# Performance work log

Hardware: AMD Instinct MI355X
Metric: run time of the kernel (lower is better)

Reference implementation:

```python
import jax, jax.numpy as jnp
import numpy as np

BATCH, CHANNELS, WINDOW, N_PATCHES = 16, 64, 200, 30
D_MODEL = 256
HIDDEN = D_MODEL // 2  # 128


def setup_inputs() -> dict:
    key = jax.random.key(0)
    ks = jax.random.split(key, 7)
    s = 1.0 / np.sqrt(HIDDEN)
    return {
        "x": jax.random.normal(ks[0], (BATCH, CHANNELS, WINDOW, N_PATCHES), dtype=jnp.float32),
        "W_ih": jax.random.normal(ks[1], (4 * HIDDEN, CHANNELS), dtype=jnp.float32) * s,
        "W_hh": jax.random.normal(ks[2], (4 * HIDDEN, HIDDEN), dtype=jnp.float32) * s,
        "b_ih": jax.random.normal(ks[3], (4 * HIDDEN,), dtype=jnp.float32) * s,
        "b_hh": jax.random.normal(ks[4], (4 * HIDDEN,), dtype=jnp.float32) * s,
        "W_fc": jax.random.normal(ks[5], (CHANNELS, HIDDEN), dtype=jnp.float32) * s,
        "b_fc": jax.random.normal(ks[6], (CHANNELS,), dtype=jnp.float32) * s,
    }


def _lstm_last_h(x_seq, W_ih, W_hh, b_ih, b_hh):
    # x_seq: (N, T, C) -> final hidden state (N, H). PyTorch gate order: i, f, g, o.
    N = x_seq.shape[0]
    H = W_hh.shape[1]
    # Precompute input contribution for all timesteps: (N, T, 4H)
    xg = jnp.einsum('ntc,gc->ntg', x_seq, W_ih) + b_ih + b_hh
    xg_t = jnp.swapaxes(xg, 0, 1)  # (T, N, 4H)

    def step(carry, xt):
        h, c = carry
        gates = xt + h @ W_hh.T  # (N, 4H)
        i, f, g, o = jnp.split(gates, 4, axis=-1)
        i = jax.nn.sigmoid(i)
        f = jax.nn.sigmoid(f)
        g = jnp.tanh(g)
        o = jax.nn.sigmoid(o)
        c = f * c + i * g
        h = o * jnp.tanh(c)
        return (h, c), None

    h0 = jnp.zeros((N, H), dtype=x_seq.dtype)
    c0 = jnp.zeros((N, H), dtype=x_seq.dtype)
    (h_T, _), _ = jax.lax.scan(step, (h0, c0), xg_t)
    return h_T


def reference(x, W_ih, W_hh, b_ih, b_hh, W_fc, b_fc):
    batch, channels, window, n_patches = x.shape
    # (B, C, T, P) -> (B, P, T, C) -> (B*P, T, C): each patch is an LSTM sequence
    x_flat = jnp.transpose(x, (0, 3, 2, 1)).reshape(batch * n_patches, window, channels)
    h_last = _lstm_last_h(x_flat, W_ih, W_hh, b_ih, b_hh)  # (B*P, H)
    out = h_last @ W_fc.T + b_fc  # (B*P, C)
    return out.reshape(batch, n_patches, channels)
```

## Files before the change

### kernel.cpp

```cpp
#include <hip/hip_runtime.h>

#define BATCH 16
#define CH    64
#define TLEN  200
#define NP    30
#define HID   128
#define NSEQ  (BATCH * NP)
#define ROWF  200

typedef _Float16 half8 __attribute__((ext_vector_type(8)));
typedef float    f32x4 __attribute__((ext_vector_type(4)));

__device__ __forceinline__ float sigm_fast(float x) {
    return __builtin_amdgcn_rcpf(1.0f + __expf(-x));
}
__device__ __forceinline__ float tanh_fast(float x) {
    float xc = fminf(15.0f, fmaxf(-15.0f, x));
    float e = __expf(2.0f * xc);
    return (e - 1.0f) * __builtin_amdgcn_rcpf(e + 1.0f);
}

#define MFMA16(A, B, C) __builtin_amdgcn_mfma_f32_16x16x32_f16((A), (B), (C), 0, 0, 0)

__global__ __launch_bounds__(512) void fused_lstm(
    const float* __restrict__ x, const float* __restrict__ W_ih,
    const float* __restrict__ W_hh, const float* __restrict__ b_ih,
    const float* __restrict__ b_hh, const float* __restrict__ W_fc,
    const float* __restrict__ b_fc, float* __restrict__ out)
{
    const int tid = threadIdx.x;
    const int w   = tid >> 6;
    const int l   = tid & 63;
    const int lr  = l & 15;
    const int lq  = l >> 4;

    const int n0 = blockIdx.x * 2;
    const int b0 = n0 / NP;
    const int p0 = n0 % NP;

    __shared__ __align__(16) _Float16 hx[2][16][ROWF];

    half8 bf[4][6];
#pragma unroll
    for (int T = 0; T < 4; ++T) {
        const int g = 128 * T + 16 * w + lr;
#pragma unroll
        for (int kt = 0; kt < 6; ++kt) {
            const int k0 = 32 * kt + 8 * lq;
            const float* src = (kt < 4) ? (W_hh + (size_t)g * HID + k0)
                                        : (W_ih + (size_t)g * CH + (k0 - 128));
            float4 f0 = *(const float4*)src;
            float4 f1 = *(const float4*)(src + 4);
            bf[T][kt] = (half8){(_Float16)f0.x, (_Float16)f0.y, (_Float16)f0.z, (_Float16)f0.w,
                                (_Float16)f1.x, (_Float16)f1.y, (_Float16)f1.z, (_Float16)f1.w};
        }
    }

    float bi, bff, bg, bo;
    {
        const int gb = 16 * w + lr;
        bi  = b_ih[gb]       + b_hh[gb];
        bff = b_ih[gb + 128] + b_hh[gb + 128];
        bg  = b_ih[gb + 256] + b_hh[gb + 256];
        bo  = b_ih[gb + 384] + b_hh[gb + 384];
    }

    const bool isload = (l >= 32 && l < 48);
    int ls = 0, lc = 0;
    const float* xptr = nullptr;
    float x0v = 0.f, xa = 0.f, xb = 0.f;
    if (isload) {
        const int idx = w * 16 + (l - 32);
        ls = idx >> 6;
        lc = idx & 63;
        xptr = x + ((size_t)(b0 * CH + lc) * TLEN) * NP + (p0 + ls);
        x0v = xptr[0];
    }

    for (int i = tid; i < 2 * 16 * ROWF / 2; i += 512) ((unsigned*)hx)[i] = 0u;
    __syncthreads();
    if (isload) {
        hx[0][ls][128 + lc] = (_Float16)x0v;
        xa = xptr[(size_t)1 * NP];
        xb = xptr[(size_t)2 * NP];
    }
    float cst = 0.f;
    __syncthreads();

    auto step = [&](int t, int cur, int nxt, float& xr) {
        const _Float16* hrow = &hx[cur][lr][8 * lq];
        half8 a0 = *(const half8*)(hrow);
        half8 a1 = *(const half8*)(hrow + 32);
        half8 a2 = *(const half8*)(hrow + 64);
        half8 a3 = *(const half8*)(hrow + 96);
        half8 a4 = *(const half8*)(hrow + 128);
        half8 a5 = *(const half8*)(hrow + 160);
        f32x4 ai = {bi,  bi,  bi,  bi };
        f32x4 af = {bff, bff, bff, bff};
        f32x4 ag = {bg,  bg,  bg,  bg };
        f32x4 ao = {bo,  bo,  bo,  bo };
#define MM4(A, KT)                                                      \
        ai = MFMA16(A, bf[0][KT], ai); af = MFMA16(A, bf[1][KT], af);   \
        ag = MFMA16(A, bf[2][KT], ag); ao = MFMA16(A, bf[3][KT], ao);
        MM4(a0, 0) MM4(a1, 1) MM4(a2, 2) MM4(a3, 3) MM4(a4, 4) MM4(a5, 5)
#undef MM4
        float gi1 = __shfl_up(ai[1], 16);
        float gf1 = __shfl_up(af[1], 16);
        float gg1 = __shfl_up(ag[1], 16);
        float go1 = __shfl_up(ao[1], 16);
        if (l < 32) {
            const bool lo = (l < 16);
            float gi = lo ? ai[0] : gi1;
            float gf = lo ? af[0] : gf1;
            float gg = lo ? ag[0] : gg1;
            float go = lo ? ao[0] : go1;
            cst = sigm_fast(gf) * cst + sigm_fast(gi) * tanh_fast(gg);
            float hv = sigm_fast(go) * tanh_fast(cst);
            hx[nxt][lq][16 * w + lr] = (_Float16)hv;
        } else if (l < 48) {
            hx[nxt][ls][128 + lc] = (_Float16)xr;
            int tn = t + 3; if (tn > TLEN - 1) tn = TLEN - 1;
            xr = xptr[(size_t)tn * NP];
        }
        __syncthreads();
    };

#pragma unroll 1
    for (int t = 0; t < TLEN; t += 2) {
        step(t,     0, 1, xa);
        step(t + 1, 1, 0, xb);
    }

    if (tid < 2 * CH) {
        const int s = tid >> 6, ch = tid & 63;
        const float* wf = W_fc + (size_t)ch * HID;
        float acc = b_fc[ch];
#pragma unroll
        for (int j8 = 0; j8 < 16; ++j8) {
            half8 hv = *(const half8*)&hx[0][s][8 * j8];
            float4 w0 = *(const float4*)(wf + 8 * j8);
            float4 w1 = *(const float4*)(wf + 8 * j8 + 4);
            acc += w0.x * (float)hv[0] + w0.y * (float)hv[1]
                 + w0.z * (float)hv[2] + w0.w * (float)hv[3]
                 + w1.x * (float)hv[4] + w1.y * (float)hv[5]
                 + w1.z * (float)hv[6] + w1.w * (float)hv[7];
        }
        out[(size_t)(n0 + s) * CH + ch] = acc;
    }
}

extern "C" void kernel_launch(void* const* d_in, const int* in_sizes, int n_in,
                              void* d_out, int out_size, void* d_ws, size_t ws_size,
                              hipStream_t stream) {
    (void)in_sizes; (void)n_in; (void)out_size; (void)d_ws; (void)ws_size;
    fused_lstm<<<NSEQ / 2, 512, 0, stream>>>(
        (const float*)d_in[0], (const float*)d_in[1], (const float*)d_in[2],
        (const float*)d_in[3], (const float*)d_in[4], (const float*)d_in[5],
        (const float*)d_in[6], (float*)d_out);
}
```

Measured before the change: 205.8 us.

## Precompute input-gate projections in 8-step chunks overlapped with recurrence

Removes the input projection (W_ih·x) from the per-step critical MFMA chain. That projection is now computed for 8 future timesteps at once, one MFMA spread across each of the 8 recurrent steps, and stored as fp16 in a double-buffered shared array. Each recurrent step now runs 16 MFMAs instead of 24. The gate pre-activation is then assembled by adding the stored values. In exchange it adds shared-memory traffic, stores the input contribution and bias in fp16 (a precision loss), and makes buffer indexing more complex.

```diff
diff --git a/kernel.cpp b/kernel.cpp
--- a/kernel.cpp
+++ b/kernel.cpp
@@ -6,10 +6,12 @@
 #define NP    30
 #define HID   128
 #define NSEQ  (BATCH * NP)
-#define ROWF  200
-
-typedef _Float16 half8 __attribute__((ext_vector_type(8)));
-typedef float    f32x4 __attribute__((ext_vector_type(4)));
+#define HXP   136
+#define XBP   72
+
+typedef _Float16 half8  __attribute__((ext_vector_type(8)));
+typedef _Float16 half2v __attribute__((ext_vector_type(2)));
+typedef float    f32x4  __attribute__((ext_vector_type(4)));
 
 __device__ __forceinline__ float sigm_fast(float x) {
     return __builtin_amdgcn_rcpf(1.0f + __expf(-x));
@@ -19,8 +21,12 @@
     float e = __expf(2.0f * xc);
     return (e - 1.0f) * __builtin_amdgcn_rcpf(e + 1.0f);
 }
-
-#define MFMA16(A, B, C) __builtin_amdgcn_mfma_f32_16x16x32_f16((A), (B), (C), 0, 0, 0)
+__device__ __forceinline__ half8 cvt8(float4 a, float4 b) {
+    return (half8){(_Float16)a.x,(_Float16)a.y,(_Float16)a.z,(_Float16)a.w,
+                   (_Float16)b.x,(_Float16)b.y,(_Float16)b.z,(_Float16)b.w};
+}
+
+#define MFMA16(A,B,C) __builtin_amdgcn_mfma_f32_16x16x32_f16((A),(B),(C),0,0,0)
 
 __global__ __launch_bounds__(512) void fused_lstm(
     const float* __restrict__ x, const float* __restrict__ W_ih,
@@ -29,106 +35,155 @@
     const float* __restrict__ b_fc, float* __restrict__ out)
 {
     const int tid = threadIdx.x;
-    const int w   = tid >> 6;
-    const int l   = tid & 63;
-    const int lr  = l & 15;
-    const int lq  = l >> 4;
+    const int w  = tid >> 6;
+    const int l  = tid & 63;
+    const int lr = l & 15;
+    const int lq = l >> 4;
 
     const int n0 = blockIdx.x * 2;
     const int b0 = n0 / NP;
     const int p0 = n0 % NP;
 
-    __shared__ __align__(16) _Float16 hx[2][16][ROWF];
-
-    half8 bf[4][6];
+    __shared__ __align__(16) _Float16 hx2[2][16][HXP];
+    __shared__ __align__(16) _Float16 xbuf[2][16][XBP];
+    __shared__ __align__(16) _Float16 xgb[2][8][HID][8];
+
+    half8 bhh[4][4];
+    half8 bih[4][2];
 #pragma unroll
     for (int T = 0; T < 4; ++T) {
-        const int g = 128 * T + 16 * w + lr;
-#pragma unroll
-        for (int kt = 0; kt < 6; ++kt) {
-            const int k0 = 32 * kt + 8 * lq;
-            const float* src = (kt < 4) ? (W_hh + (size_t)g * HID + k0)
-                                        : (W_ih + (size_t)g * CH + (k0 - 128));
-            float4 f0 = *(const float4*)src;
-            float4 f1 = *(const float4*)(src + 4);
-            bf[T][kt] = (half8){(_Float16)f0.x, (_Float16)f0.y, (_Float16)f0.z, (_Float16)f0.w,
-                                (_Float16)f1.x, (_Float16)f1.y, (_Float16)f1.z, (_Float16)f1.w};
-        }
-    }
-
-    float bi, bff, bg, bo;
+        const int g = 128*T + 16*w + lr;
+        const float* rh = W_hh + (size_t)g * HID;
+        const float* ri = W_ih + (size_t)g * CH;
+#pragma unroll
+        for (int kt = 0; kt < 4; ++kt) {
+            const int k0 = 32*kt + 8*lq;
+            bhh[T][kt] = cvt8(*(const float4*)(rh + k0), *(const float4*)(rh + k0 + 4));
+        }
+#pragma unroll
+        for (int j = 0; j < 2; ++j) {
+            const int k0 = 32*j + 8*lq;
+            bih[T][j] = cvt8(*(const float4*)(ri + k0), *(const float4*)(ri + k0 + 4));
+        }
+    }
+    float bias0, bias1, bias2, bias3;
     {
-        const int gb = 16 * w + lr;
-        bi  = b_ih[gb]       + b_hh[gb];
-        bff = b_ih[gb + 128] + b_hh[gb + 128];
-        bg  = b_ih[gb + 256] + b_hh[gb + 256];
-        bo  = b_ih[gb + 384] + b_hh[gb + 384];
-    }
-
-    const bool isload = (l >= 32 && l < 48);
+        const int gb = 16*w + lr;
+        bias0 = b_ih[gb]       + b_hh[gb];
+        bias1 = b_ih[gb + 128] + b_hh[gb + 128];
+        bias2 = b_ih[gb + 256] + b_hh[gb + 256];
+        bias3 = b_ih[gb + 384] + b_hh[gb + 384];
+    }
+
+    for (int i = tid; i < (2*16*HXP)/2; i += 512) ((unsigned*)hx2)[i] = 0u;
+
+    const bool isload = (l >= 16 && l < 32);
     int ls = 0, lc = 0;
-    const float* xptr = nullptr;
-    float x0v = 0.f, xa = 0.f, xb = 0.f;
+    const float* xbase = nullptr;
+    float xpend = 0.f;
+    f32x4 xga0, xga1, xga2, xga3;
+    half8 xf0, xf1;
     if (isload) {
-        const int idx = w * 16 + (l - 32);
+        const int idx = w * 16 + (l - 16);
         ls = idx >> 6;
         lc = idx & 63;
-        xptr = x + ((size_t)(b0 * CH + lc) * TLEN) * NP + (p0 + ls);
-        x0v = xptr[0];
-    }
-
-    for (int i = tid; i < 2 * 16 * ROWF / 2; i += 512) ((unsigned*)hx)[i] = 0u;
+        xbase = x + ((size_t)(b0 * CH + lc) * TLEN) * NP + p0 + ls;
+#pragma unroll
+        for (int u = 0; u < 16; ++u)
+            xbuf[u >> 3][2*(u & 7) + ls][lc] = (_Float16)xbase[(size_t)u * NP];
+        xpend = xbase[(size_t)16 * NP];
+    }
+    float c0 = 0.f, c1 = 0.f;
     __syncthreads();
-    if (isload) {
-        hx[0][ls][128 + lc] = (_Float16)x0v;
-        xa = xptr[(size_t)1 * NP];
-        xb = xptr[(size_t)2 * NP];
-    }
-    float cst = 0.f;
+
+#define WRITE_XGA(BUF) {                                                          \
+        _Float16* q0_ = &xgb[BUF][2*lq][16*w + lr][0];                            \
+        _Float16* q1_ = &xgb[BUF][2*lq + 1][16*w + lr][0];                        \
+        *(half2v*)(q0_ + 0) = (half2v){(_Float16)xga0[0], (_Float16)xga1[0]};     \
+        *(half2v*)(q0_ + 2) = (half2v){(_Float16)xga2[0], (_Float16)xga3[0]};     \
+        *(half2v*)(q0_ + 4) = (half2v){(_Float16)xga0[1], (_Float16)xga1[1]};     \
+        *(half2v*)(q0_ + 6) = (half2v){(_Float16)xga2[1], (_Float16)xga3[1]};     \
+        *(half2v*)(q1_ + 0) = (half2v){(_Float16)xga0[2], (_Float16)xga1[2]};     \
+        *(half2v*)(q1_ + 2) = (half2v){(_Float16)xga2[2], (_Float16)xga3[2]};     \
+        *(half2v*)(q1_ + 4) = (half2v){(_Float16)xga0[3], (_Float16)xga1[3]};     \
+        *(half2v*)(q1_ + 6) = (half2v){(_Float16)xga2[3], (_Float16)xga3[3]}; }
+
+    {
+        const _Float16* xr = &xbuf[0][lr][8 * lq];
+        xf0 = *(const half8*)xr;
+        xf1 = *(const half8*)(xr + 32);
+        xga0 = (f32x4){bias0, bias0, bias0, bias0};
+        xga1 = (f32x4){bias1, bias1, bias1, bias1};
+        xga2 = (f32x4){bias2, bias2, bias2, bias2};
+        xga3 = (f32x4){bias3, bias3, bias3, bias3};
+        xga0 = MFMA16(xf0, bih[0][0], xga0); xga0 = MFMA16(xf1, bih[0][1], xga0);
+        xga1 = MFMA16(xf0, bih[1][0], xga1); xga1 = MFMA16(xf1, bih[1][1], xga1);
+        xga2 = MFMA16(xf0, bih[2][0], xga2); xga2 = MFMA16(xf1, bih[2][1], xga2);
+        xga3 = MFMA16(xf0, bih[3][0], xga3); xga3 = MFMA16(xf1, bih[3][1], xga3);
+        WRITE_XGA(0)
+    }
     __syncthreads();
 
-    auto step = [&](int t, int cur, int nxt, float& xr) {
-        const _Float16* hrow = &hx[cur][lr][8 * lq];
-        half8 a0 = *(const half8*)(hrow);
-        half8 a1 = *(const half8*)(hrow + 32);
-        half8 a2 = *(const half8*)(hrow + 64);
-        half8 a3 = *(const half8*)(hrow + 96);
-        half8 a4 = *(const half8*)(hrow + 128);
-        half8 a5 = *(const half8*)(hrow + 160);
-        f32x4 ai = {bi,  bi,  bi,  bi };
-        f32x4 af = {bff, bff, bff, bff};
-        f32x4 ag = {bg,  bg,  bg,  bg };
-        f32x4 ao = {bo,  bo,  bo,  bo };
-#define MM4(A, KT)                                                      \
-        ai = MFMA16(A, bf[0][KT], ai); af = MFMA16(A, bf[1][KT], af);   \
-        ag = MFMA16(A, bf[2][KT], ag); ao = MFMA16(A, bf[3][KT], ao);
-        MM4(a0, 0) MM4(a1, 1) MM4(a2, 2) MM4(a3, 3) MM4(a4, 4) MM4(a5, 5)
-#undef MM4
-        float gi1 = __shfl_up(ai[1], 16);
-        float gf1 = __shfl_up(af[1], 16);
-        float gg1 = __shfl_up(ag[1], 16);
-        float go1 = __shfl_up(ao[1], 16);
-        if (l < 32) {
-            const bool lo = (l < 16);
-            float gi = lo ? ai[0] : gi1;
-            float gf = lo ? af[0] : gf1;
-            float gg = lo ? ag[0] : gg1;
-            float go = lo ? ao[0] : go1;
-            cst = sigm_fast(gf) * cst + sigm_fast(gi) * tanh_fast(gg);
-            float hv = sigm_fast(go) * tanh_fast(cst);
-            hx[nxt][lq][16 * w + lr] = (_Float16)hv;
-        } else if (l < 48) {
-            hx[nxt][ls][128 + lc] = (_Float16)xr;
-            int tn = t + 3; if (tn > TLEN - 1) tn = TLEN - 1;
-            xr = xptr[(size_t)tn * NP];
-        }
-        __syncthreads();
-    };
+#define MM4(A, KT)                                                       \
+        ci = MFMA16(A, bhh[0][KT], ci); cf = MFMA16(A, bhh[1][KT], cf);  \
+        cg = MFMA16(A, bhh[2][KT], cg); co = MFMA16(A, bhh[3][KT], co);
 
 #pragma unroll 1
-    for (int t = 0; t < TLEN; t += 2) {
-        step(t,     0, 1, xa);
-        step(t + 1, 1, 0, xb);
+    for (int p = 0; p < 25; ++p) {
+        const int pe = p & 1;
+#pragma unroll
+        for (int k = 0; k < 8; ++k) {
+            const int cur = k & 1;
+            const int nxt = cur ^ 1;
+            if (k == 0) {
+                const _Float16* xr = &xbuf[pe ^ 1][lr][8 * lq];
+                xf0 = *(const half8*)xr;
+                xf1 = *(const half8*)(xr + 32);
+                xga0 = (f32x4){bias0, bias0, bias0, bias0};
+                xga1 = (f32x4){bias1, bias1, bias1, bias1};
+                xga2 = (f32x4){bias2, bias2, bias2, bias2};
+                xga3 = (f32x4){bias3, bias3, bias3, bias3};
+            }
+            const _Float16* hr = &hx2[cur][lr][8 * lq];
+            half8 a0 = *(const half8*)(hr);
+            half8 a1 = *(const half8*)(hr + 32);
+            half8 a2 = *(const half8*)(hr + 64);
+            half8 a3 = *(const half8*)(hr + 96);
+            f32x4 ci = {0.f, 0.f, 0.f, 0.f};
+            f32x4 cf = ci, cg = ci, co = ci;
+            MM4(a0, 0) MM4(a1, 1) MM4(a2, 2) MM4(a3, 3)
+            if (k == 0) xga0 = MFMA16(xf0, bih[0][0], xga0);
+            if (k == 1) xga0 = MFMA16(xf1, bih[0][1], xga0);
+            if (k == 2) xga1 = MFMA16(xf0, bih[1][0], xga1);
+            if (k == 3) xga1 = MFMA16(xf1, bih[1][1], xga1);
+            if (k == 4) xga2 = MFMA16(xf0, bih[2][0], xga2);
+            if (k == 5) xga2 = MFMA16(xf1, bih[2][1], xga2);
+            if (k == 6) xga3 = MFMA16(xf0, bih[3][0], xga3);
+            if (k == 7) xga3 = MFMA16(xf1, bih[3][1], xga3);
+
+            if (l < 16) {
+                half8 xgv = *(const half8*)&xgb[pe][k][16*w + lr][0];
+                float gi0 = ci[0] + (float)xgv[0];
+                float gf0 = cf[0] + (float)xgv[1];
+                float gg0 = cg[0] + (float)xgv[2];
+                float go0 = co[0] + (float)xgv[3];
+                float gi1 = ci[1] + (float)xgv[4];
+                float gf1 = cf[1] + (float)xgv[5];
+                float gg1 = cg[1] + (float)xgv[6];
+                float go1 = co[1] + (float)xgv[7];
+                c0 = sigm_fast(gf0) * c0 + sigm_fast(gi0) * tanh_fast(gg0);
+                c1 = sigm_fast(gf1) * c1 + sigm_fast(gi1) * tanh_fast(gg1);
+                hx2[nxt][0][16*w + lr] = (_Float16)(sigm_fast(go0) * tanh_fast(c0));
+                hx2[nxt][1][16*w + lr] = (_Float16)(sigm_fast(go1) * tanh_fast(c1));
+            } else if (l < 32) {
+                xbuf[pe][2*k + ls][lc] = (_Float16)xpend;
+                int tq = 8*p + k + 17;
+                tq = tq > TLEN - 1 ? TLEN - 1 : tq;
+                xpend = xbase[(size_t)tq * NP];
+            }
+            if (k == 7) WRITE_XGA(pe ^ 1)
+            __syncthreads();
+        }
     }
 
     if (tid < 2 * CH) {
@@ -137,7 +192,7 @@
         float acc = b_fc[ch];
 #pragma unroll
         for (int j8 = 0; j8 < 16; ++j8) {
-            half8 hv = *(const half8*)&hx[0][s][8 * j8];
+            half8 hv = *(const half8*)&hx2[0][s][8 * j8];
             float4 w0 = *(const float4*)(wf + 8 * j8);
             float4 w1 = *(const float4*)(wf + 8 * j8 + 4);
             acc += w0.x * (float)hv[0] + w0.y * (float)hv[1]
```

Measured after the change: 226.0 us. +9.8%, slower.
